# Optimization experiments

Hardware: AMD Instinct MI355X
Metric: run time of the kernel (lower is better)

The kernel has to match this reference:

```python
import jax, jax.numpy as jnp
from jax import lax
import numpy as np

N_BASIS = 256
N_FREQ = 128
N_TIME = 8
LAM = 0.2
LR = 1e-3
B1, B2, EPS = 0.9, 0.999, 1e-8
CONV_TOL = 1e-3


def setup_inputs() -> dict:
    key = jax.random.key(0)
    k1, k2 = jax.random.split(key)
    spec = jax.random.normal(k1, (32, N_FREQ, 256), dtype=jnp.float32)
    basis = jax.random.normal(k2, (N_FREQ * N_TIME, N_BASIS), dtype=jnp.float32)
    return {"spec": spec, "basis": basis, "n_iter_coef": 30, "pad": 0, "stride": 4}


def normalize01(x):
    # torch normalize01 with dims=-1, keepdims
    xmin = x.min(axis=-1, keepdims=True)
    xmax = x.max(axis=-1, keepdims=True)
    return (x - xmin) / (xmax - xmin)


def _response(x, basis, n_iter):
    # x: [B, D]; Adam-optimize coef [B, N_BASIS] for n_iter steps with the
    # same early-stop rule as the torch code (frozen via a done flag).
    B = x.shape[0]
    sig = jnp.std(x, ddof=1)  # torch .std() is unbiased over all elements

    def loss_fn(coef):
        pred = coef @ basis.T                      # [B, D]
        mse = jnp.mean((pred - x) ** 2)
        return mse + LAM * sig * jnp.mean(jnp.abs(coef / sig))

    coef0 = jnp.full((B, N_BASIS), 0.5 / N_BASIS, dtype=jnp.float32)
    m0 = jnp.zeros_like(coef0)
    v0 = jnp.zeros_like(coef0)

    def body(carry, _):
        coef, m, v, t, old_loss, done = carry
        loss, g = jax.value_and_grad(loss_fn)(coef)
        t_new = t + 1.0
        m_new = B1 * m + (1.0 - B1) * g
        v_new = B2 * v + (1.0 - B2) * g * g
        mhat = m_new / (1.0 - B1 ** t_new)
        vhat = v_new / (1.0 - B2 ** t_new)
        coef_new = coef - LR * mhat / (jnp.sqrt(vhat) + EPS)
        conv = jnp.abs(old_loss - loss) / old_loss < CONV_TOL
        sel = lambda a, b: jnp.where(done, a, b)
        new_carry = (
            sel(coef, coef_new),
            sel(m, m_new),
            sel(v, v_new),
            jnp.where(done, t, t_new),
            jnp.where(done, old_loss, loss),
            done | conv,
        )
        return new_carry, None

    init = (coef0, m0, v0, jnp.float32(0.0), jnp.float32(1e-10), jnp.array(False))
    (coef, _, _, _, _, _), _ = lax.scan(body, init, None, length=n_iter)
    return coef  # detached in torch


def reference(spec, basis, n_iter_coef, pad, stride):
    if spec.ndim == 2:
        spec = spec[None, ...]
    B, F, T = spec.shape
    spec_ = jnp.pad(spec, ((0, 0), (0, 0), (pad, pad)))
    starts = np.arange(0, T - N_TIME + 1, stride)          # window start frames
    idx = starts[:, None] + np.arange(N_TIME)              # [W, N_TIME]
    wins = spec_[:, :, idx]                                # [B, F, W, N_TIME]
    x = jnp.transpose(wins, (2, 0, 1, 3)).reshape(len(starts), B, F * N_TIME)
    x = normalize01(x)                                     # per row of [B, D]
    coef = jax.vmap(lambda xw: _response(xw, basis, n_iter_coef))(x)  # [W, B, N_BASIS]
    return jnp.transpose(coef, (1, 2, 0))                  # [B, N_BASIS, W]
```

## Files before the change

kernel.cpp:

```cpp
#include <hip/hip_runtime.h>
#include <math.h>

#define NB     256
#define NF     128
#define FT     1024
#define NW     63
#define TORIG  256
#define MAXIT  48
#define RPB    8
#define NBLK   4
#define GRID   256

#define SW_S 292
#define SW_M 36
#define SW_SZ (7*SW_S + 7*SW_M + 7*4 + 4)

__device__ __forceinline__ float rl(float v, int lane) {
    return __uint_as_float((unsigned)__builtin_amdgcn_readlane((int)__float_as_uint(v), lane));
}

__global__ __launch_bounds__(512, 2) void window_kernel(
    const float* __restrict__ spec,
    const float* __restrict__ basis,
    float* __restrict__ G,
    const int* __restrict__ p_niter,
    const int* __restrict__ p_pad,
    const int* __restrict__ p_stride,
    double* __restrict__ sxbuf,
    double* __restrict__ gpart,
    unsigned int* __restrict__ gcnt,
    float* __restrict__ out)
{
    __shared__ float  s_part[RPB * RPB * 64 * 4];
    __shared__ float  s_xn[RPB * FT];
    __shared__ float  s_cf[SW_SZ];
    __shared__ float  s_cf2[RPB][NB];
    __shared__ float  s_gred[2][NB];
    __shared__ float  s_mn[RPB], s_rng[RPB];
    __shared__ float  s_red[8][2];
    __shared__ double s_dred[8];
    __shared__ int    s_stop;

    const int bid    = blockIdx.x;
    const int yy     = bid >> 3;
    const int q      = yy & 3;
    const int w      = (bid & 7) + 8 * (yy >> 2);
    const int tid    = threadIdx.x;
    const int ks     = tid >> 6;
    const int kg     = tid & 63;
    const int n_iter = p_niter[0];
    const int t0     = w * p_stride[0] - p_pad[0];
    unsigned int* gbar = gcnt + MAXIT * NW;

    {
        const int r = bid;
        const int c = tid & 255, jh = tid >> 8;
        float acc = 0.f;
        const float* bp = basis + (size_t)(jh * 512) * NB;
        #pragma unroll 16
        for (int j = 0; j < 512; ++j)
            acc = fmaf(bp[j * NB + r], bp[j * NB + c], acc);
        s_gred[jh][c] = acc;
        __syncthreads();
        if (jh == 0) G[(size_t)r * NB + c] = s_gred[0][c] + s_gred[1][c];
    }
    __threadfence();
    __syncthreads();
    if (tid == 0) atomicAdd(gbar, 1u);

    if (w >= NW) return;

    #pragma unroll
    for (int i = 0; i < 16; ++i) {
        const int e = i * 512 + tid;
        const int b = e >> 10, jj = e & 1023;
        const int f = jj >> 3, t = jj & 7, tq = t0 + t;
        s_xn[b * FT + jj] = (tq >= 0 && tq < TORIG)
            ? spec[((size_t)(q * RPB + b) * NF + f) * TORIG + tq] : 0.f;
    }
    __syncthreads();
    {
        float mn = __builtin_inff(), mx = -__builtin_inff();
        #pragma unroll
        for (int i = 0; i < 16; ++i) {
            const float v = s_xn[ks * FT + i * 64 + kg];
            mn = fminf(mn, v); mx = fmaxf(mx, v);
        }
        #pragma unroll
        for (int off = 32; off; off >>= 1) {
            mn = fminf(mn, __shfl_down(mn, off));
            mx = fmaxf(mx, __shfl_down(mx, off));
        }
        if (kg == 0) { s_mn[ks] = mn; s_rng[ks] = mx - mn; }
    }
    __syncthreads();
    double sx2p = 0.0;
    #pragma unroll
    for (int i = 0; i < 16; ++i) {
        const int e = i * 512 + tid;
        const int b = e >> 10, jj = e & 1023;
        const float v = (s_xn[b * FT + jj] - s_mn[b]) / s_rng[b];
        s_xn[b * FT + jj] = v;
        sx2p += (double)v * (double)v;
    }
    #pragma unroll
    for (int off = 32; off; off >>= 1) sx2p += __shfl_down(sx2p, off);
    if (kg == 0) s_dred[ks] = sx2p;
    __syncthreads();
    if (tid == 0) {
        double s = 0.0;
        #pragma unroll
        for (int i = 0; i < 8; ++i) s += s_dred[i];
        sxbuf[w * NBLK + q] = s;
    }

    float xbp[RPB][4];
    #pragma unroll
    for (int b = 0; b < RPB; ++b)
        #pragma unroll
        for (int j = 0; j < 4; ++j) xbp[b][j] = 0.f;
    for (int i0 = 0; i0 < 128; i0 += 4) {
        const int jj = ks * 128 + i0;
        float4 bv[4];
        #pragma unroll
        for (int t = 0; t < 4; ++t)
            bv[t] = *(const float4*)(basis + (size_t)(jj + t) * NB + 4 * kg);
        #pragma unroll
        for (int b = 0; b < RPB; ++b) {
            const float4 x4 = *(const float4*)&s_xn[b * FT + jj];
            xbp[b][0] = fmaf(x4.x, bv[0].x, fmaf(x4.y, bv[1].x, fmaf(x4.z, bv[2].x, fmaf(x4.w, bv[3].x, xbp[b][0]))));
            xbp[b][1] = fmaf(x4.x, bv[0].y, fmaf(x4.y, bv[1].y, fmaf(x4.z, bv[2].y, fmaf(x4.w, bv[3].y, xbp[b][1]))));
            xbp[b][2] = fmaf(x4.x, bv[0].z, fmaf(x4.y, bv[1].z, fmaf(x4.z, bv[2].z, fmaf(x4.w, bv[3].z, xbp[b][2]))));
            xbp[b][3] = fmaf(x4.x, bv[0].w, fmaf(x4.y, bv[1].w, fmaf(x4.z, bv[2].w, fmaf(x4.w, bv[3].w, xbp[b][3]))));
        }
    }
    #pragma unroll
    for (int b = 0; b < RPB; ++b)
        *(float4*)&s_part[((ks * RPB + b) * 64 + kg) * 4] =
            make_float4(xbp[b][0], xbp[b][1], xbp[b][2], xbp[b][3]);
    __syncthreads();
    float xB[4] = {0.f, 0.f, 0.f, 0.f};
    #pragma unroll
    for (int k2 = 0; k2 < 8; ++k2) {
        const float4 p4 = *(const float4*)&s_part[((k2 * RPB + ks) * 64 + kg) * 4];
        xB[0] += p4.x; xB[1] += p4.y; xB[2] += p4.z; xB[3] += p4.w;
    }

    if (tid == 0) {
        while (__hip_atomic_load(gbar, __ATOMIC_ACQUIRE, __HIP_MEMORY_SCOPE_AGENT) < (unsigned)GRID)
            __builtin_amdgcn_s_sleep(1);
    }
    __syncthreads();
    float4 g[32];
    #pragma unroll
    for (int kl = 0; kl < 32; ++kl)
        g[kl] = *(const float4*)(G + (size_t)(32 * ks + kl) * NB + 4 * kg);

    const float C0 = 0.5f / 256.f;
    float cf[4] = {C0, C0, C0, C0}, m_[4] = {0, 0, 0, 0}, v_[4] = {0, 0, 0, 0};
    *(float4*)&s_cf[(kg >> 3) * SW_S + (kg & 7) * SW_M + ks * 4] = make_float4(C0, C0, C0, C0);
    *(float4*)&s_cf2[ks][4 * kg] = make_float4(C0, C0, C0, C0);
    if (tid == 0) s_stop = 0;
    float b1p = 1.f, b2p = 1.f;
    float old_loss = 1e-10f;
    double sxtot = 0.0;
    const float c1 = 2.f / 32768.f, c2 = 0.2f / 8192.f;

    for (int it = 0; it < n_iter; ++it) {
        __syncthreads();

        if (tid == 64) {
            int stop = 0;
            if (it > 0) {
                const size_t pbm = ((size_t)(it - 1) * NW + w) * NBLK;
                while (__hip_atomic_load(&gcnt[(it - 1) * NW + w], __ATOMIC_ACQUIRE,
                                         __HIP_MEMORY_SCOPE_AGENT) < (unsigned)NBLK)
                    __builtin_amdgcn_s_sleep(1);
                double Qt = 0.0, Rt = 0.0;
                #pragma unroll
                for (int i = 0; i < NBLK; ++i) {
                    Qt += gpart[(pbm + i) * 2 + 0];
                    Rt += gpart[(pbm + i) * 2 + 1];
                }
                if (it == 1)
                    sxtot = sxbuf[w * NBLK + 0] + sxbuf[w * NBLK + 1] +
                            sxbuf[w * NBLK + 2] + sxbuf[w * NBLK + 3];
                const float loss = (float)((Qt + sxtot) / 32768.0 + 0.2 * (Rt / 8192.0));
                const float stat = fabsf(old_loss - loss) / old_loss;
                old_loss = loss;
                stop = (stat < 1e-3f) ? 1 : 0;
            }
            s_stop = stop;
        }

        const float4 c4 = *(const float4*)&s_cf[ks * SW_S + (kg >> 3) * SW_M + (kg & 7) * 4];
        float pacc[RPB][4];
        #pragma unroll
        for (int b = 0; b < RPB; ++b)
            #pragma unroll
            for (int j = 0; j < 4; ++j) pacc[b][j] = 0.f;
        #pragma unroll
        for (int m = 0; m < 8; ++m) {
            const float4 ga = g[4 * m + 0], gb = g[4 * m + 1];
            const float4 gc = g[4 * m + 2], gd = g[4 * m + 3];
            #pragma unroll
            for (int b = 0; b < RPB; ++b) {
                const int L = m * 8 + b;
                const float cx = rl(c4.x, L), cy = rl(c4.y, L);
                const float cz = rl(c4.z, L), cw = rl(c4.w, L);
                pacc[b][0] = fmaf(cx, ga.x, fmaf(cy, gb.x, fmaf(cz, gc.x, fmaf(cw, gd.x, pacc[b][0]))));
                pacc[b][1] = fmaf(cx, ga.y, fmaf(cy, gb.y, fmaf(cz, gc.y, fmaf(cw, gd.y, pacc[b][1]))));
                pacc[b][2] = fmaf(cx, ga.z, fmaf(cy, gb.z, fmaf(cz, gc.z, fmaf(cw, gd.z, pacc[b][2]))));
                pacc[b][3] = fmaf(cx, ga.w, fmaf(cy, gb.w, fmaf(cz, gc.w, fmaf(cw, gd.w, pacc[b][3]))));
            }
        }

        float qc = 0.f, rr = 0.f;
        #pragma unroll
        for (int b = 0; b < RPB; ++b) {
            const float4 cc = *(const float4*)&s_cf2[b][4 * kg];
            qc += pacc[b][0] * cc.x + pacc[b][1] * cc.y +
                  pacc[b][2] * cc.z + pacc[b][3] * cc.w;
        }
        #pragma unroll
        for (int j = 0; j < 4; ++j) {
            qc -= 2.f * cf[j] * xB[j];
            rr += fabsf(cf[j]);
        }

        #pragma unroll
        for (int b = 0; b < RPB; ++b)
            *(float4*)&s_part[((ks * RPB + b) * 64 + kg) * 4] =
                make_float4(pacc[b][0], pacc[b][1], pacc[b][2], pacc[b][3]);

        #pragma unroll
        for (int off = 32; off; off >>= 1) {
            qc += __shfl_down(qc, off);
            rr += __shfl_down(rr, off);
        }
        if (kg == 0) { s_red[ks][0] = qc; s_red[ks][1] = rr; }

        __syncthreads();

        if (s_stop) break;

        if (tid == 0) {
            float Q = 0.f, R = 0.f;
            #pragma unroll
            for (int i = 0; i < 8; ++i) { Q += s_red[i][0]; R += s_red[i][1]; }
            const size_t pb = ((size_t)it * NW + w) * NBLK;
            gpart[(pb + q) * 2 + 0] = (double)Q;
            gpart[(pb + q) * 2 + 1] = (double)R;
            __hip_atomic_fetch_add(&gcnt[it * NW + w], 1u,
                                   __ATOMIC_RELEASE, __HIP_MEMORY_SCOPE_AGENT);
        }

        float a4[4] = {0.f, 0.f, 0.f, 0.f};
        #pragma unroll
        for (int k2 = 0; k2 < 8; ++k2) {
            const float4 p4 = *(const float4*)&s_part[((k2 * RPB + ks) * 64 + kg) * 4];
            a4[0] += p4.x; a4[1] += p4.y; a4[2] += p4.z; a4[3] += p4.w;
        }

        b1p *= 0.9f; b2p *= 0.999f;
        const float bc1 = 1.f - b1p, bc2 = 1.f - b2p;
        #pragma unroll
        for (int j = 0; j < 4; ++j) {
            const float c_ = cf[j];
            const float sgn = (c_ > 0.f) ? 1.f : ((c_ < 0.f) ? -1.f : 0.f);
            const float gg = c1 * (a4[j] - xB[j]) + c2 * sgn;
            m_[j] = 0.9f * m_[j] + 0.1f * gg;
            v_[j] = 0.999f * v_[j] + 0.001f * gg * gg;
            cf[j] = c_ - 1e-3f * (m_[j] / bc1) / (sqrtf(v_[j] / bc2) + 1e-8f);
        }
        *(float4*)&s_cf[(kg >> 3) * SW_S + (kg & 7) * SW_M + ks * 4] =
            make_float4(cf[0], cf[1], cf[2], cf[3]);
        *(float4*)&s_cf2[ks][4 * kg] = make_float4(cf[0], cf[1], cf[2], cf[3]);
    }

    #pragma unroll
    for (int j = 0; j < 4; ++j)
        out[((size_t)(q * RPB + ks) * NB + 4 * kg + j) * NW + w] = cf[j];
}

extern "C" void kernel_launch(void* const* d_in, const int* in_sizes, int n_in,
                              void* d_out, int out_size, void* d_ws, size_t ws_size,
                              hipStream_t stream)
{
    const float* spec   = (const float*)d_in[0];
    const float* basis  = (const float*)d_in[1];
    const int* p_niter  = (const int*)d_in[2];
    const int* p_pad    = (const int*)d_in[3];
    const int* p_stride = (const int*)d_in[4];
    float* out = (float*)d_out;

    char* ws = (char*)d_ws;
    float*        G     = (float*)ws;
    double*       sxbuf = (double*)(ws + 262144);
    double*       gpart = (double*)(ws + 262144 + 4096);
    unsigned int* gcnt  = (unsigned int*)(ws + 262144 + 4096 + 193536);

    hipMemsetAsync(gcnt, 0, (MAXIT * NW + 1) * sizeof(unsigned int), stream);
    window_kernel<<<dim3(GRID), dim3(512), 0, stream>>>(
        spec, basis, G, p_niter, p_pad, p_stride, sxbuf, gpart, gcnt, out);
}
```

Baseline: 343.0 us.

## Double-buffer partial sums, drop per-iteration barrier and use global double atomics for loss

Restructures the Adam iteration loop so each thread's coefficients come straight from registers via readlane, with no shared-memory coefficient copies. Partial products are double-buffered in shared memory so only one barrier per iteration is needed. The loss quadratic term is rewritten using the reduced gradient products, which removes the extra dot pass against the coefficients. Per-wave double atomicAdds into global buffers replace per-block partial slots and the block-level reduction, at the cost of more global atomics and a nondeterministic summation order.

Measured after the change: 925.6 us. 2.7x slower.

```diff
diff --git a/kernel.cpp b/kernel.cpp
--- a/kernel.cpp
+++ b/kernel.cpp
@@ -9,11 +9,8 @@
 #define MAXIT  48
 #define RPB    8
 #define NBLK   4
+#define NARR   (8 * NBLK)
 #define GRID   256
-
-#define SW_S 292
-#define SW_M 36
-#define SW_SZ (7*SW_S + 7*SW_M + 7*4 + 4)
 
 __device__ __forceinline__ float rl(float v, int lane) {
     return __uint_as_float((unsigned)__builtin_amdgcn_readlane((int)__float_as_uint(v), lane));
@@ -27,47 +24,46 @@
     const int* __restrict__ p_pad,
     const int* __restrict__ p_stride,
     double* __restrict__ sxbuf,
-    double* __restrict__ gpart,
+    double* __restrict__ gq,
+    double* __restrict__ gr_,
     unsigned int* __restrict__ gcnt,
     float* __restrict__ out)
 {
-    __shared__ float  s_part[RPB * RPB * 64 * 4];
-    __shared__ float  s_xn[RPB * FT];
-    __shared__ float  s_cf[SW_SZ];
-    __shared__ float  s_cf2[RPB][NB];
+    __shared__ float  s_p0[RPB * RPB * 256];
+    __shared__ float  s_p1[RPB * RPB * 256];
     __shared__ float  s_gred[2][NB];
     __shared__ float  s_mn[RPB], s_rng[RPB];
-    __shared__ float  s_red[8][2];
     __shared__ double s_dred[8];
-    __shared__ int    s_stop;
-
-    const int bid    = blockIdx.x;
-    const int yy     = bid >> 3;
-    const int q      = yy & 3;
-    const int w      = (bid & 7) + 8 * (yy >> 2);
-    const int tid    = threadIdx.x;
-    const int ks     = tid >> 6;
-    const int kg     = tid & 63;
+    __shared__ int    s_stop[2];
+    float* const s_xn = s_p1;
+
+    const int bid = blockIdx.x;
+    const int yy  = bid >> 3;
+    const int q   = yy & 3;
+    const int w   = (bid & 7) + 8 * (yy >> 2);
+    const int tid = threadIdx.x;
+    const int ks  = tid >> 6;
+    const int kg  = tid & 63;
+    const int r   = kg >> 3;
+    const int c0  = 32 * ks + 4 * (kg & 7);
     const int n_iter = p_niter[0];
     const int t0     = w * p_stride[0] - p_pad[0];
     unsigned int* gbar = gcnt + MAXIT * NW;
 
     {
-        const int r = bid;
         const int c = tid & 255, jh = tid >> 8;
         float acc = 0.f;
         const float* bp = basis + (size_t)(jh * 512) * NB;
         #pragma unroll 16
         for (int j = 0; j < 512; ++j)
-            acc = fmaf(bp[j * NB + r], bp[j * NB + c], acc);
+            acc = fmaf(bp[j * NB + bid], bp[j * NB + c], acc);
         s_gred[jh][c] = acc;
         __syncthreads();
-        if (jh == 0) G[(size_t)r * NB + c] = s_gred[0][c] + s_gred[1][c];
+        if (jh == 0) G[(size_t)bid * NB + c] = s_gred[0][c] + s_gred[1][c];
     }
     __threadfence();
     __syncthreads();
     if (tid == 0) atomicAdd(gbar, 1u);
-
     if (w >= NW) return;
 
     #pragma unroll
@@ -134,15 +130,16 @@
             xbp[b][3] = fmaf(x4.x, bv[0].w, fmaf(x4.y, bv[1].w, fmaf(x4.z, bv[2].w, fmaf(x4.w, bv[3].w, xbp[b][3]))));
         }
     }
+    __syncthreads();
     #pragma unroll
     for (int b = 0; b < RPB; ++b)
-        *(float4*)&s_part[((ks * RPB + b) * 64 + kg) * 4] =
+        *(float4*)&s_p0[(ks * RPB + b) * 256 + 4 * kg] =
             make_float4(xbp[b][0], xbp[b][1], xbp[b][2], xbp[b][3]);
     __syncthreads();
     float xB[4] = {0.f, 0.f, 0.f, 0.f};
     #pragma unroll
     for (int k2 = 0; k2 < 8; ++k2) {
-        const float4 p4 = *(const float4*)&s_part[((k2 * RPB + ks) * 64 + kg) * 4];
+        const float4 p4 = *(const float4*)&s_p0[(k2 * RPB + r) * 256 + c0];
         xB[0] += p4.x; xB[1] += p4.y; xB[2] += p4.z; xB[3] += p4.w;
     }
 
@@ -158,42 +155,31 @@
 
     const float C0 = 0.5f / 256.f;
     float cf[4] = {C0, C0, C0, C0}, m_[4] = {0, 0, 0, 0}, v_[4] = {0, 0, 0, 0};
-    *(float4*)&s_cf[(kg >> 3) * SW_S + (kg & 7) * SW_M + ks * 4] = make_float4(C0, C0, C0, C0);
-    *(float4*)&s_cf2[ks][4 * kg] = make_float4(C0, C0, C0, C0);
-    if (tid == 0) s_stop = 0;
+    if (tid == 64) { s_stop[0] = 0; s_stop[1] = 0; }
     float b1p = 1.f, b2p = 1.f;
     float old_loss = 1e-10f;
     double sxtot = 0.0;
     const float c1 = 2.f / 32768.f, c2 = 0.2f / 8192.f;
 
     for (int it = 0; it < n_iter; ++it) {
-        __syncthreads();
-
-        if (tid == 64) {
-            int stop = 0;
-            if (it > 0) {
-                const size_t pbm = ((size_t)(it - 1) * NW + w) * NBLK;
-                while (__hip_atomic_load(&gcnt[(it - 1) * NW + w], __ATOMIC_ACQUIRE,
-                                         __HIP_MEMORY_SCOPE_AGENT) < (unsigned)NBLK)
-                    __builtin_amdgcn_s_sleep(1);
-                double Qt = 0.0, Rt = 0.0;
-                #pragma unroll
-                for (int i = 0; i < NBLK; ++i) {
-                    Qt += gpart[(pbm + i) * 2 + 0];
-                    Rt += gpart[(pbm + i) * 2 + 1];
-                }
-                if (it == 1)
-                    sxtot = sxbuf[w * NBLK + 0] + sxbuf[w * NBLK + 1] +
-                            sxbuf[w * NBLK + 2] + sxbuf[w * NBLK + 3];
-                const float loss = (float)((Qt + sxtot) / 32768.0 + 0.2 * (Rt / 8192.0));
-                const float stat = fabsf(old_loss - loss) / old_loss;
-                old_loss = loss;
-                stop = (stat < 1e-3f) ? 1 : 0;
-            }
-            s_stop = stop;
-        }
-
-        const float4 c4 = *(const float4*)&s_cf[ks * SW_S + (kg >> 3) * SW_M + (kg & 7) * 4];
+        const int p = it & 1;
+        float* const sp = p ? s_p1 : s_p0;
+
+        if (tid == 64 && it > 0) {
+            while (__hip_atomic_load(&gcnt[(it - 1) * NW + w], __ATOMIC_ACQUIRE,
+                                     __HIP_MEMORY_SCOPE_AGENT) < (unsigned)NARR)
+                __builtin_amdgcn_s_sleep(1);
+            const double Qt = gq[(it - 1) * NW + w];
+            const double Rt = gr_[(it - 1) * NW + w];
+            if (it == 1)
+                sxtot = sxbuf[w * NBLK + 0] + sxbuf[w * NBLK + 1] +
+                        sxbuf[w * NBLK + 2] + sxbuf[w * NBLK + 3];
+            const float loss = (float)((Qt + sxtot) / 32768.0 + 0.2 * (Rt / 8192.0));
+            const float stat = fabsf(old_loss - loss) / old_loss;
+            old_loss = loss;
+            s_stop[p] = (stat < 1e-3f) ? 1 : 0;
+        }
+
         float pacc[RPB][4];
         #pragma unroll
         for (int b = 0; b < RPB; ++b)
@@ -205,61 +191,47 @@
             const float4 gc = g[4 * m + 2], gd = g[4 * m + 3];
             #pragma unroll
             for (int b = 0; b < RPB; ++b) {
-                const int L = m * 8 + b;
-                const float cx = rl(c4.x, L), cy = rl(c4.y, L);
-                const float cz = rl(c4.z, L), cw = rl(c4.w, L);
+                const int L = b * 8 + m;
+                const float cx = rl(cf[0], L), cy = rl(cf[1], L);
+                const float cz = rl(cf[2], L), cw = rl(cf[3], L);
                 pacc[b][0] = fmaf(cx, ga.x, fmaf(cy, gb.x, fmaf(cz, gc.x, fmaf(cw, gd.x, pacc[b][0]))));
                 pacc[b][1] = fmaf(cx, ga.y, fmaf(cy, gb.y, fmaf(cz, gc.y, fmaf(cw, gd.y, pacc[b][1]))));
                 pacc[b][2] = fmaf(cx, ga.z, fmaf(cy, gb.z, fmaf(cz, gc.z, fmaf(cw, gd.z, pacc[b][2]))));
                 pacc[b][3] = fmaf(cx, ga.w, fmaf(cy, gb.w, fmaf(cz, gc.w, fmaf(cw, gd.w, pacc[b][3]))));
             }
         }
+        #pragma unroll
+        for (int b = 0; b < RPB; ++b)
+            *(float4*)&sp[(ks * RPB + b) * 256 + 4 * kg] =
+                make_float4(pacc[b][0], pacc[b][1], pacc[b][2], pacc[b][3]);
+
+        __syncthreads();
+
+        if (s_stop[p]) break;
+
+        float a4[4] = {0.f, 0.f, 0.f, 0.f};
+        #pragma unroll
+        for (int k2 = 0; k2 < 8; ++k2) {
+            const float4 p4 = *(const float4*)&sp[(k2 * RPB + r) * 256 + c0];
+            a4[0] += p4.x; a4[1] += p4.y; a4[2] += p4.z; a4[3] += p4.w;
+        }
 
         float qc = 0.f, rr = 0.f;
         #pragma unroll
-        for (int b = 0; b < RPB; ++b) {
-            const float4 cc = *(const float4*)&s_cf2[b][4 * kg];
-            qc += pacc[b][0] * cc.x + pacc[b][1] * cc.y +
-                  pacc[b][2] * cc.z + pacc[b][3] * cc.w;
-        }
-        #pragma unroll
         for (int j = 0; j < 4; ++j) {
-            qc -= 2.f * cf[j] * xB[j];
+            qc += cf[j] * (a4[j] - 2.f * xB[j]);
             rr += fabsf(cf[j]);
         }
-
-        #pragma unroll
-        for (int b = 0; b < RPB; ++b)
-            *(float4*)&s_part[((ks * RPB + b) * 64 + kg) * 4] =
-                make_float4(pacc[b][0], pacc[b][1], pacc[b][2], pacc[b][3]);
-
         #pragma unroll
         for (int off = 32; off; off >>= 1) {
             qc += __shfl_down(qc, off);
             rr += __shfl_down(rr, off);
         }
-        if (kg == 0) { s_red[ks][0] = qc; s_red[ks][1] = rr; }
-
-        __syncthreads();
-
-        if (s_stop) break;
-
-        if (tid == 0) {
-            float Q = 0.f, R = 0.f;
-            #pragma unroll
-            for (int i = 0; i < 8; ++i) { Q += s_red[i][0]; R += s_red[i][1]; }
-            const size_t pb = ((size_t)it * NW + w) * NBLK;
-            gpart[(pb + q) * 2 + 0] = (double)Q;
-            gpart[(pb + q) * 2 + 1] = (double)R;
+        if (kg == 0) {
+            atomicAdd(&gq[it * NW + w], (double)qc);
+            atomicAdd(&gr_[it * NW + w], (double)rr);
             __hip_atomic_fetch_add(&gcnt[it * NW + w], 1u,
                                    __ATOMIC_RELEASE, __HIP_MEMORY_SCOPE_AGENT);
-        }
-
-        float a4[4] = {0.f, 0.f, 0.f, 0.f};
-        #pragma unroll
-        for (int k2 = 0; k2 < 8; ++k2) {
-            const float4 p4 = *(const float4*)&s_part[((k2 * RPB + ks) * 64 + kg) * 4];
-            a4[0] += p4.x; a4[1] += p4.y; a4[2] += p4.z; a4[3] += p4.w;
         }
 
         b1p *= 0.9f; b2p *= 0.999f;
@@ -273,14 +245,11 @@
             v_[j] = 0.999f * v_[j] + 0.001f * gg * gg;
             cf[j] = c_ - 1e-3f * (m_[j] / bc1) / (sqrtf(v_[j] / bc2) + 1e-8f);
         }
-        *(float4*)&s_cf[(kg >> 3) * SW_S + (kg & 7) * SW_M + ks * 4] =
-            make_float4(cf[0], cf[1], cf[2], cf[3]);
-        *(float4*)&s_cf2[ks][4 * kg] = make_float4(cf[0], cf[1], cf[2], cf[3]);
     }
 
     #pragma unroll
     for (int j = 0; j < 4; ++j)
-        out[((size_t)(q * RPB + ks) * NB + 4 * kg + j) * NW + w] = cf[j];
+        out[((size_t)(q * RPB + r) * NB + c0 + j) * NW + w] = cf[j];
 }
 
 extern "C" void kernel_launch(void* const* d_in, const int* in_sizes, int n_in,
@@ -297,10 +266,11 @@
     char* ws = (char*)d_ws;
     float*        G     = (float*)ws;
     double*       sxbuf = (double*)(ws + 262144);
-    double*       gpart = (double*)(ws + 262144 + 4096);
-    unsigned int* gcnt  = (unsigned int*)(ws + 262144 + 4096 + 193536);
-
-    hipMemsetAsync(gcnt, 0, (MAXIT * NW + 1) * sizeof(unsigned int), stream);
+    double*       gq    = (double*)(ws + 266240);
+    double*       gr_   = (double*)(ws + 290816);
+    unsigned int* gcnt  = (unsigned int*)(ws + 315392);
+
+    hipMemsetAsync(ws + 266240, 0, 24576 + 24576 + 12100 + 28, stream);
     window_kernel<<<dim3(GRID), dim3(512), 0, stream>>>(
-        spec, basis, G, p_niter, p_pad, p_stride, sxbuf, gpart, gcnt, out);
+        spec, basis, G, p_niter, p_pad, p_stride, sxbuf, gq, gr_, gcnt, out);
 }
```
